# Optimization experiments

Measured on AMD Instinct MI355X. Metric: run time of the kernel, lower is better.

## Reference

```python
import jax, jax.numpy as jnp
import numpy as np

HID, HEADS = 1024, 16
HEAD_DIM = HID // HEADS

def _rope_table(seq_len, d):
    inv_freq = 1.0 / (10000.0 ** (jnp.arange(0, d, 2, dtype=jnp.float32) / d))  # [d/2]
    sin_inp = jnp.arange(seq_len, dtype=jnp.float32)[:, None] * inv_freq[None, :]  # [S, d/2]
    return jnp.concatenate([jnp.sin(sin_inp), jnp.cos(sin_inp)], axis=-1)  # [S, d]

def _apply_rope(x, pos_emb):
    # Faithful to original: cos/sin of the (already sin/cos) pos_emb values.
    half = x.shape[-1] // 2
    x1, x2 = x[..., :half], x[..., half:]
    p1, p2 = pos_emb[..., :half], pos_emb[..., half:]
    return jnp.concatenate([x1 * jnp.cos(p1) + x2 * jnp.sin(p1),
                            x2 * jnp.cos(p2) - x1 * jnp.sin(p2)], axis=-1)

def setup_inputs() -> dict:
    key = jax.random.key(0)
    ks = jax.random.split(key, 11)
    B, S = 8, 1024
    s = 1.0 / np.sqrt(HID)
    return {
        'query': jax.random.normal(ks[0], (B, S, HID), jnp.float32),
        'key':   jax.random.normal(ks[1], (B, S, HID), jnp.float32),
        'value': jax.random.normal(ks[2], (B, S, HID), jnp.float32),
        'Wq': jax.random.normal(ks[3], (HID, HID), jnp.float32) * s,
        'bq': jax.random.normal(ks[4], (HID,), jnp.float32) * s,
        'Wk': jax.random.normal(ks[5], (HID, HID), jnp.float32) * s,
        'bk': jax.random.normal(ks[6], (HID,), jnp.float32) * s,
        'Wv': jax.random.normal(ks[7], (HID, HID), jnp.float32) * s,
        'bv': jax.random.normal(ks[8], (HID,), jnp.float32) * s,
        'Wo': jax.random.normal(ks[9], (HID, HID), jnp.float32) * s,
        'bo': jax.random.normal(ks[10], (HID,), jnp.float32) * s,
    }

def reference(query, key, value, Wq, bq, Wk, bk, Wv, bv, Wo, bo):
    B, S, _ = query.shape
    q = query @ Wq.T + bq
    k = key @ Wk.T + bk
    v = value @ Wv.T + bv
    pos_emb = _rope_table(S, HID)
    q = _apply_rope(q, pos_emb)
    k = _apply_rope(k, pos_emb)
    v = _apply_rope(v, pos_emb)  # original applies RoPE to V too
    # split heads: [B, H, S, D]
    q = q.reshape(B, S, HEADS, HEAD_DIM).transpose(0, 2, 1, 3)
    k = k.reshape(B, S, HEADS, HEAD_DIM).transpose(0, 2, 1, 3)
    v = v.reshape(B, S, HEADS, HEAD_DIM).transpose(0, 2, 1, 3)
    scale = jnp.sqrt(jnp.float32(HEAD_DIM))
    attn = jnp.einsum('bhqd,bhkd->bhqk', q, k) / scale
    attn = jax.nn.softmax(attn, axis=-1)  # dropout=0.0 (eval): identity
    x = jnp.einsum('bhqk,bhkd->bhqd', attn, v)
    x = x.transpose(0, 2, 1, 3).reshape(B, S, HID)
    return x @ Wo.T + bo
```

## Files before the change

### kernel.cpp

```cpp
#include <hip/hip_runtime.h>
#include <hip/hip_fp16.h>
#include <cmath>


typedef _Float16 f16;
typedef __attribute__((ext_vector_type(4))) _Float16 f16x4;
typedef __attribute__((ext_vector_type(8))) _Float16 f16x8;
typedef __attribute__((ext_vector_type(4))) float f32x4;

#define MFMA16(a, b, c) __builtin_amdgcn_mfma_f32_16x16x32_f16((a), (b), (c), 0, 0, 0)
#define MFMA16K16(a, b, c) __builtin_amdgcn_mfma_f32_16x16x16f16((a), (b), (c), 0, 0, 0)

__device__ __forceinline__ void g2l16(void* lds, const void* g) {
  __builtin_amdgcn_global_load_lds(
      (const __attribute__((address_space(1))) void*)g,
      (__attribute__((address_space(3))) void*)lds,
      16, 0, 0);
}

__global__ void cvt3_kernel(const float* __restrict__ a, const float* __restrict__ b,
                            const float* __restrict__ c,
                            f16* __restrict__ oa, f16* __restrict__ ob, f16* __restrict__ oc) {
  const float* src;
  f16* dst;
  if (blockIdx.y == 0) { src = a; dst = oa; }
  else if (blockIdx.y == 1) { src = b; dst = ob; }
  else { src = c; dst = oc; }
  size_t t = (size_t)blockIdx.x * 256 + threadIdx.x;
  float4 v = ((const float4*)src)[t];
  f16x4 w = { (f16)v.x, (f16)v.y, (f16)v.z, (f16)v.w };
  ((f16x4*)dst)[t] = w;
}

__global__ void cvt4_kernel(const float* __restrict__ a, const float* __restrict__ b,
                            const float* __restrict__ c, const float* __restrict__ d,
                            f16* __restrict__ oa, f16* __restrict__ ob,
                            f16* __restrict__ oc, f16* __restrict__ od) {
  const float* src;
  f16* dst;
  if (blockIdx.y == 0) { src = a; dst = oa; }
  else if (blockIdx.y == 1) { src = b; dst = ob; }
  else if (blockIdx.y == 2) { src = c; dst = oc; }
  else { src = d; dst = od; }
  size_t t = (size_t)blockIdx.x * 256 + threadIdx.x;
  float4 v = ((const float4*)src)[t];
  f16x4 w = { (f16)v.x, (f16)v.y, (f16)v.z, (f16)v.w };
  ((f16x4*)dst)[t] = w;
}

struct GemmBatch {
  const f16* A[3];
  const f16* W[3];
  const float* bias[3];
  void* O[3];
};

template <bool OUT_F16>
__global__ __launch_bounds__(256)
void gemm_f16_kernel(GemmBatch gb) {
  __shared__ __align__(16) f16 sA[128 * 64];
  __shared__ __align__(16) f16 sB[128 * 64];
  const int z = blockIdx.z;
  const f16* __restrict__ A = gb.A[z];
  const f16* __restrict__ Bw = gb.W[z];
  const float* __restrict__ bias = gb.bias[z];
  void* __restrict__ Out = gb.O[z];

  const int tid = threadIdx.x;
  const int lane = tid & 63;
  const int wv = tid >> 6;
  const int l15 = lane & 15;
  const int quad = lane >> 4;
  const int m0 = blockIdx.y * 128;
  const int n0 = blockIdx.x * 128;

  const int srow = lane >> 3;
  const int schunk = (lane & 7) ^ srow;
  const int wm = (wv & 1) * 64;
  const int wn = (wv >> 1) * 64;

  const f16* gA = A + (size_t)(m0 + wv * 32 + srow) * 1024 + schunk * 8;
  const f16* gB = Bw + (size_t)(n0 + wv * 32 + srow) * 1024 + schunk * 8;
  f16* lA = sA + (wv * 32) * 64;
  f16* lB = sB + (wv * 32) * 64;

  f32x4 acc[4][4] = {};

  for (int k0 = 0; k0 < 1024; k0 += 64) {
    __syncthreads();
#pragma unroll
    for (int j = 0; j < 4; ++j) {
      g2l16(lA + j * 8 * 64, gA + (size_t)j * 8 * 1024 + k0);
      g2l16(lB + j * 8 * 64, gB + (size_t)j * 8 * 1024 + k0);
    }
    __syncthreads();
#pragma unroll
    for (int kc = 0; kc < 2; ++kc) {
      f16x8 af[4], bf[4];
#pragma unroll
      for (int t = 0; t < 4; ++t) {
        const int swz = ((kc * 4 + quad) ^ (l15 & 7)) * 8;
        af[t] = *(const f16x8*)(sA + (wm + t * 16 + l15) * 64 + swz);
        bf[t] = *(const f16x8*)(sB + (wn + t * 16 + l15) * 64 + swz);
      }
#pragma unroll
      for (int mi = 0; mi < 4; ++mi)
#pragma unroll
        for (int ni = 0; ni < 4; ++ni)
          acc[mi][ni] = MFMA16(af[mi], bf[ni], acc[mi][ni]);
    }
  }

#pragma unroll
  for (int ni = 0; ni < 4; ++ni) {
    const int col = n0 + wn + ni * 16 + l15;
    const float bv = bias[col];
#pragma unroll
    for (int mi = 0; mi < 4; ++mi) {
      const int row0 = m0 + wm + mi * 16 + quad * 4;
#pragma unroll
      for (int r = 0; r < 4; ++r) {
        float v = acc[mi][ni][r] + bv;
        if (OUT_F16)
          ((f16*)Out)[(size_t)(row0 + r) * 1024 + col] = (f16)v;
        else
          ((float*)Out)[(size_t)(row0 + r) * 1024 + col] = v;
      }
    }
  }
}

__global__ __launch_bounds__(256)
void rope_kernel(f16* __restrict__ q, f16* __restrict__ k,
                 const f16* __restrict__ v, f16* __restrict__ vt) {
  __shared__ f16 sT[128 * 72];
  const int t = threadIdx.x;
  const int c0 = blockIdx.x * 64;
  const int s0 = blockIdx.y * 64;
  const int b = blockIdx.z;
  const int sr = t >> 2;
  const int cq = (t & 3) * 16;
  const int s = s0 + sr;

  float c1[16], s1[16], c2[16], s2[16];
#pragma unroll
  for (int j = 0; j < 16; ++j) {
    const int i = c0 + cq + j;
    const float invf = exp2f((float)i * -0.025952563241307517f);
    const float th = (float)s * invf;
    const float p1 = sinf(th), p2 = cosf(th);
    c1[j] = __cosf(p1); s1[j] = __sinf(p1);
    c2[j] = __cosf(p2); s2[j] = __sinf(p2);
  }

  const size_t base = ((size_t)(b * 1024 + s)) * 1024 + c0 + cq;

#pragma unroll
  for (int tz = 0; tz < 2; ++tz) {
    f16* ptr = tz ? k : q;
    f16x8 x1a = *(f16x8*)(ptr + base);
    f16x8 x1b = *(f16x8*)(ptr + base + 8);
    f16x8 x2a = *(f16x8*)(ptr + base + 512);
    f16x8 x2b = *(f16x8*)(ptr + base + 520);
    f16x8 r1a, r1b, r2a, r2b;
#pragma unroll
    for (int j = 0; j < 8; ++j) {
      float a0 = (float)x1a[j], b0 = (float)x2a[j];
      float a1 = (float)x1b[j], b1 = (float)x2b[j];
      r1a[j] = (f16)(a0 * c1[j] + b0 * s1[j]);
      r2a[j] = (f16)(b0 * c2[j] - a0 * s2[j]);
      r1b[j] = (f16)(a1 * c1[8 + j] + b1 * s1[8 + j]);
      r2b[j] = (f16)(b1 * c2[8 + j] - a1 * s2[8 + j]);
    }
    *(f16x8*)(ptr + base) = r1a;
    *(f16x8*)(ptr + base + 8) = r1b;
    *(f16x8*)(ptr + base + 512) = r2a;
    *(f16x8*)(ptr + base + 520) = r2b;
  }

  {
    f16x8 x1a = *(const f16x8*)(v + base);
    f16x8 x1b = *(const f16x8*)(v + base + 8);
    f16x8 x2a = *(const f16x8*)(v + base + 512);
    f16x8 x2b = *(const f16x8*)(v + base + 520);
#pragma unroll
    for (int j = 0; j < 8; ++j) {
      float a0 = (float)x1a[j], b0 = (float)x2a[j];
      float a1 = (float)x1b[j], b1 = (float)x2b[j];
      sT[(cq + j) * 72 + sr] = (f16)(a0 * c1[j] + b0 * s1[j]);
      sT[(64 + cq + j) * 72 + sr] = (f16)(b0 * c2[j] - a0 * s2[j]);
      sT[(cq + 8 + j) * 72 + sr] = (f16)(a1 * c1[8 + j] + b1 * s1[8 + j]);
      sT[(64 + cq + 8 + j) * 72 + sr] = (f16)(b1 * c2[8 + j] - a1 * s2[8 + j]);
    }
  }
  __syncthreads();

  const int lr = t >> 1;
  const int sh = (t & 1) * 32;
  const int h = (lr < 64) ? (c0 >> 6) : (8 + (c0 >> 6));
  const int d = lr & 63;
  const size_t gbase = ((size_t)((b * 16 + h) * 64 + d)) * 1024 + s0 + sh;
#pragma unroll
  for (int m = 0; m < 4; ++m)
    *(f16x8*)(vt + gbase + m * 8) = *(const f16x8*)(sT + lr * 72 + sh + m * 8);
}

__global__ __launch_bounds__(256)
void attn_kernel(const f16* __restrict__ q, const f16* __restrict__ k,
                 const f16* __restrict__ vt, f16* __restrict__ xo) {
  __shared__ __align__(16) f16 sK[128 * 64];
  __shared__ __align__(16) f16 sV[64 * 128];
  const int tid = threadIdx.x;
  const int lane = tid & 63;
  const int wv = tid >> 6;
  const int l15 = lane & 15;
  const int quad = lane >> 4;
  const int bh = blockIdx.x;
  const int qt = blockIdx.y;
  const int b = bh >> 4, h = bh & 15;
  const size_t hidbase = ((size_t)b << 20) + (size_t)(h << 6);
  const int sq0 = qt * 128 + wv * 32;

  f16x8 fq[2][2];
#pragma unroll
  for (int mi = 0; mi < 2; ++mi)
#pragma unroll
    for (int kc = 0; kc < 2; ++kc)
      fq[mi][kc] = *(const f16x8*)(q + hidbase + (size_t)(sq0 + mi * 16 + l15) * 1024 +
                                   kc * 32 + quad * 8);

  f32x4 ot[2][4] = {};
  float lrun[2] = {};

  const float SC = 0.18033688011112042f;

  const int srowK = lane >> 3;
  const int schunkK = (lane & 7) ^ srowK;
  const f16* gK = k + hidbase + (size_t)(wv * 32 + srowK) * 1024 + schunkK * 8;
  const int vrow = lane >> 4;
  const f16* gVbase = vt + ((size_t)bh * 64) * 1024;

  for (int kt = 0; kt < 8; ++kt) {
    const int sk0 = kt * 128;
    __syncthreads();
#pragma unroll
    for (int j = 0; j < 4; ++j)
      g2l16(sK + (wv * 32 + j * 8) * 64, gK + (size_t)(sk0 + j * 8) * 1024);
#pragma unroll
    for (int i = 0; i < 4; ++i) {
      const int row = wv * 16 + i * 4 + vrow;
      const int gch = (lane & 15) ^ (i * 4 + vrow);
      g2l16(sV + (wv * 16 + i * 4) * 128, gVbase + (size_t)row * 1024 + sk0 + gch * 8);
    }
    __syncthreads();

#pragma unroll
    for (int nj = 0; nj < 8; ++nj) {
      f32x4 st[2] = {};
#pragma unroll
      for (int kc = 0; kc < 2; ++kc) {
        f16x8 fk = *(const f16x8*)(sK + (nj * 16 + l15) * 64 +
                                   ((kc * 4 + quad) ^ (l15 & 7)) * 8);
        st[0] = MFMA16(fk, fq[0][kc], st[0]);
        st[1] = MFMA16(fk, fq[1][kc], st[1]);
      }
      f16x4 pf[2];
#pragma unroll
      for (int mi = 0; mi < 2; ++mi) {
#pragma unroll
        for (int r = 0; r < 4; ++r) {
          float p = exp2f(fmaf(st[mi][r], SC, -12.0f));
          lrun[mi] += p;
          pf[mi][r] = (f16)p;
        }
      }
#pragma unroll
      for (int nd = 0; nd < 4; ++nd) {
        f16x4 fv = *(const f16x4*)(sV + (nd * 16 + l15) * 128 +
                                   ((nj * 2 + (quad >> 1)) ^ l15) * 8 + (quad & 1) * 4);
        ot[0][nd] = MFMA16K16(fv, pf[0], ot[0][nd]);
        ot[1][nd] = MFMA16K16(fv, pf[1], ot[1][nd]);
      }
    }
  }

  float inv[2];
#pragma unroll
  for (int mi = 0; mi < 2; ++mi) {
    float l = lrun[mi];
    l += __shfl_xor(l, 16, 64);
    l += __shfl_xor(l, 32, 64);
    inv[mi] = 1.0f / l;
  }

  __syncthreads();
  f16* sO = sK + wv * (32 * 72);
#pragma unroll
  for (int mi = 0; mi < 2; ++mi)
#pragma unroll
    for (int nd = 0; nd < 4; ++nd) {
      f16x4 w;
#pragma unroll
      for (int r = 0; r < 4; ++r) w[r] = (f16)(ot[mi][nd][r] * inv[mi]);
      *(f16x4*)(sO + (mi * 16 + l15) * 72 + nd * 16 + quad * 4) = w;
    }
  const int orow = lane >> 1;
  const int ocol = (lane & 1) * 32;
  const size_t gb = hidbase + (size_t)(sq0 + orow) * 1024 + ocol;
#pragma unroll
  for (int m = 0; m < 4; ++m)
    *(f16x8*)(xo + gb + m * 8) = *(const f16x8*)(sO + orow * 72 + ocol + m * 8);
}

extern "C" void kernel_launch(void* const* d_in, const int* in_sizes, int n_in,
                              void* d_out, int out_size, void* d_ws, size_t ws_size,
                              hipStream_t stream) {
  const float* query = (const float*)d_in[0];
  const float* key   = (const float*)d_in[1];
  const float* value = (const float*)d_in[2];
  const float* Wq = (const float*)d_in[3];
  const float* bq = (const float*)d_in[4];
  const float* Wk = (const float*)d_in[5];
  const float* bk = (const float*)d_in[6];
  const float* Wv = (const float*)d_in[7];
  const float* bv = (const float*)d_in[8];
  const float* Wo = (const float*)d_in[9];
  const float* bo = (const float*)d_in[10];

  char* ws = (char*)d_ws;
  const size_t SZT = (size_t)8 * 1024 * 1024 * 2;
  const size_t SZW = (size_t)1024 * 1024 * 2;
  f16* Xq  = (f16*)(ws);
  f16* Xk  = (f16*)(ws + SZT);
  f16* Xv  = (f16*)(ws + 2 * SZT);
  f16* Wqh = (f16*)(ws + 3 * SZT);
  f16* Wkh = (f16*)(ws + 3 * SZT + SZW);
  f16* Wvh = (f16*)(ws + 3 * SZT + 2 * SZW);
  f16* Woh = (f16*)(ws + 3 * SZT + 3 * SZW);
  f16* Qp  = (f16*)(ws + 3 * SZT + 4 * SZW);
  f16* Kp  = (f16*)(ws + 4 * SZT + 4 * SZW);
  f16* Vp  = (f16*)(ws + 5 * SZT + 4 * SZW);
  f16* Vt  = (f16*)(ws + 6 * SZT + 4 * SZW);
  f16* Xat = (f16*)(ws + 7 * SZT + 4 * SZW);

  cvt3_kernel<<<dim3(8192, 3), 256, 0, stream>>>(query, key, value, Xq, Xk, Xv);
  cvt4_kernel<<<dim3(1024, 4), 256, 0, stream>>>(Wq, Wk, Wv, Wo, Wqh, Wkh, Wvh, Woh);

  GemmBatch gqkv;
  gqkv.A[0] = Xq;  gqkv.A[1] = Xk;  gqkv.A[2] = Xv;
  gqkv.W[0] = Wqh; gqkv.W[1] = Wkh; gqkv.W[2] = Wvh;
  gqkv.bias[0] = bq; gqkv.bias[1] = bk; gqkv.bias[2] = bv;
  gqkv.O[0] = Qp;  gqkv.O[1] = Kp;  gqkv.O[2] = Vp;
  gemm_f16_kernel<true><<<dim3(8, 64, 3), 256, 0, stream>>>(gqkv);

  rope_kernel<<<dim3(8, 16, 8), 256, 0, stream>>>(Qp, Kp, Vp, Vt);

  attn_kernel<<<dim3(128, 8), 256, 0, stream>>>(Qp, Kp, Vt, Xat);

  GemmBatch go;
  go.A[0] = Xat; go.A[1] = nullptr; go.A[2] = nullptr;
  go.W[0] = Woh; go.W[1] = nullptr; go.W[2] = nullptr;
  go.bias[0] = bo; go.bias[1] = nullptr; go.bias[2] = nullptr;
  go.O[0] = d_out; go.O[1] = nullptr; go.O[2] = nullptr;
  gemm_f16_kernel<false><<<dim3(8, 64, 1), 256, 0, stream>>>(go);
}
```

Baseline: 341.9 us.

## Fuse fp32-to-fp16 activation conversion into QKV GEMM and remap tiles per XCD

Removes the separate conversion kernel for query/key/value. The QKV GEMM now loads fp32 activations directly, converts them in registers and stores swizzled fp16 into LDS, which saves writing and re-reading three fp16 activation copies. It also remaps the block index so that neighbouring M tiles are grouped per XCD, aiming for better L2 reuse. The cost is that A loads become synchronous register loads instead of async global-to-LDS loads, and each A byte is fetched at twice the width from global memory for every N tile.

```diff
diff --git a/kernel.cpp b/kernel.cpp
--- a/kernel.cpp
+++ b/kernel.cpp
@@ -16,20 +16,6 @@
       (const __attribute__((address_space(1))) void*)g,
       (__attribute__((address_space(3))) void*)lds,
       16, 0, 0);
-}
-
-__global__ void cvt3_kernel(const float* __restrict__ a, const float* __restrict__ b,
-                            const float* __restrict__ c,
-                            f16* __restrict__ oa, f16* __restrict__ ob, f16* __restrict__ oc) {
-  const float* src;
-  f16* dst;
-  if (blockIdx.y == 0) { src = a; dst = oa; }
-  else if (blockIdx.y == 1) { src = b; dst = ob; }
-  else { src = c; dst = oc; }
-  size_t t = (size_t)blockIdx.x * 256 + threadIdx.x;
-  float4 v = ((const float4*)src)[t];
-  f16x4 w = { (f16)v.x, (f16)v.y, (f16)v.z, (f16)v.w };
-  ((f16x4*)dst)[t] = w;
 }
 
 __global__ void cvt4_kernel(const float* __restrict__ a, const float* __restrict__ b,
@@ -49,19 +35,19 @@
 }
 
 struct GemmBatch {
-  const f16* A[3];
+  const void* A[3];
   const f16* W[3];
   const float* bias[3];
   void* O[3];
 };
 
-template <bool OUT_F16>
+template <bool A_FP32, bool OUT_F16>
 __global__ __launch_bounds__(256)
 void gemm_f16_kernel(GemmBatch gb) {
   __shared__ __align__(16) f16 sA[128 * 64];
   __shared__ __align__(16) f16 sB[128 * 64];
   const int z = blockIdx.z;
-  const f16* __restrict__ A = gb.A[z];
+  const void* __restrict__ Araw = gb.A[z];
   const f16* __restrict__ Bw = gb.W[z];
   const float* __restrict__ bias = gb.bias[z];
   void* __restrict__ Out = gb.O[z];
@@ -71,27 +57,57 @@
   const int wv = tid >> 6;
   const int l15 = lane & 15;
   const int quad = lane >> 4;
-  const int m0 = blockIdx.y * 128;
-  const int n0 = blockIdx.x * 128;
+
+  const int flat = blockIdx.x + (blockIdx.y << 3);
+  const int xcd = flat & 7;
+  const int t64 = flat >> 3;
+  const int m0 = (xcd * 8 + (t64 & 7)) * 128;
+  const int n0 = (t64 >> 3) * 128;
+
+  const int wm = (wv & 1) * 64;
+  const int wn = (wv >> 1) * 64;
 
   const int srow = lane >> 3;
   const int schunk = (lane & 7) ^ srow;
-  const int wm = (wv & 1) * 64;
-  const int wn = (wv >> 1) * 64;
-
-  const f16* gA = A + (size_t)(m0 + wv * 32 + srow) * 1024 + schunk * 8;
   const f16* gB = Bw + (size_t)(n0 + wv * 32 + srow) * 1024 + schunk * 8;
+  f16* lB = sB + (wv * 32) * 64;
+
+  const f16* gA16 = (const f16*)Araw + (size_t)(m0 + wv * 32 + srow) * 1024 + schunk * 8;
   f16* lA = sA + (wv * 32) * 64;
-  f16* lB = sB + (wv * 32) * 64;
+  const int gi = lane >> 4, ii = lane & 15;
+  const int rowl = gi * 8 + (ii >> 1);
+  const int kh = (ii & 1) * 32;
+  const float* gA32 = (const float*)Araw + (size_t)(m0 + wv * 32 + rowl) * 1024 + kh;
+  f16* sAw = sA + (size_t)(wv * 32 + rowl) * 64;
 
   f32x4 acc[4][4] = {};
 
   for (int k0 = 0; k0 < 1024; k0 += 64) {
     __syncthreads();
 #pragma unroll
-    for (int j = 0; j < 4; ++j) {
-      g2l16(lA + j * 8 * 64, gA + (size_t)j * 8 * 1024 + k0);
+    for (int j = 0; j < 4; ++j)
       g2l16(lB + j * 8 * 64, gB + (size_t)j * 8 * 1024 + k0);
+    if constexpr (A_FP32) {
+#pragma unroll
+      for (int half = 0; half < 2; ++half) {
+        float4 va[4];
+#pragma unroll
+        for (int j = 0; j < 4; ++j)
+          va[j] = *(const float4*)(gA32 + k0 + half * 16 + j * 4);
+        const float* vf = (const float*)va;
+#pragma unroll
+        for (int c = 0; c < 2; ++c) {
+          f16x8 w;
+#pragma unroll
+          for (int e = 0; e < 8; ++e) w[e] = (f16)vf[c * 8 + e];
+          const int ch = (ii & 1) * 4 + half * 2 + c;
+          *(f16x8*)(sAw + ((ch ^ (rowl & 7)) * 8)) = w;
+        }
+      }
+    } else {
+#pragma unroll
+      for (int j = 0; j < 4; ++j)
+        g2l16(lA + j * 8 * 64, gA16 + (size_t)j * 8 * 1024 + k0);
     }
     __syncthreads();
 #pragma unroll
@@ -330,28 +346,24 @@
   char* ws = (char*)d_ws;
   const size_t SZT = (size_t)8 * 1024 * 1024 * 2;
   const size_t SZW = (size_t)1024 * 1024 * 2;
-  f16* Xq  = (f16*)(ws);
-  f16* Xk  = (f16*)(ws + SZT);
-  f16* Xv  = (f16*)(ws + 2 * SZT);
-  f16* Wqh = (f16*)(ws + 3 * SZT);
-  f16* Wkh = (f16*)(ws + 3 * SZT + SZW);
-  f16* Wvh = (f16*)(ws + 3 * SZT + 2 * SZW);
-  f16* Woh = (f16*)(ws + 3 * SZT + 3 * SZW);
-  f16* Qp  = (f16*)(ws + 3 * SZT + 4 * SZW);
-  f16* Kp  = (f16*)(ws + 4 * SZT + 4 * SZW);
-  f16* Vp  = (f16*)(ws + 5 * SZT + 4 * SZW);
-  f16* Vt  = (f16*)(ws + 6 * SZT + 4 * SZW);
-  f16* Xat = (f16*)(ws + 7 * SZT + 4 * SZW);
-
-  cvt3_kernel<<<dim3(8192, 3), 256, 0, stream>>>(query, key, value, Xq, Xk, Xv);
+  f16* Wqh = (f16*)(ws);
+  f16* Wkh = (f16*)(ws + SZW);
+  f16* Wvh = (f16*)(ws + 2 * SZW);
+  f16* Woh = (f16*)(ws + 3 * SZW);
+  f16* Qp  = (f16*)(ws + 4 * SZW);
+  f16* Kp  = (f16*)(ws + 4 * SZW + SZT);
+  f16* Vp  = (f16*)(ws + 4 * SZW + 2 * SZT);
+  f16* Vt  = (f16*)(ws + 4 * SZW + 3 * SZT);
+  f16* Xat = (f16*)(ws + 4 * SZW + 4 * SZT);
+
   cvt4_kernel<<<dim3(1024, 4), 256, 0, stream>>>(Wq, Wk, Wv, Wo, Wqh, Wkh, Wvh, Woh);
 
   GemmBatch gqkv;
-  gqkv.A[0] = Xq;  gqkv.A[1] = Xk;  gqkv.A[2] = Xv;
-  gqkv.W[0] = Wqh; gqkv.W[1] = Wkh; gqkv.W[2] = Wvh;
+  gqkv.A[0] = query; gqkv.A[1] = key; gqkv.A[2] = value;
+  gqkv.W[0] = Wqh;   gqkv.W[1] = Wkh; gqkv.W[2] = Wvh;
   gqkv.bias[0] = bq; gqkv.bias[1] = bk; gqkv.bias[2] = bv;
-  gqkv.O[0] = Qp;  gqkv.O[1] = Kp;  gqkv.O[2] = Vp;
-  gemm_f16_kernel<true><<<dim3(8, 64, 3), 256, 0, stream>>>(gqkv);
+  gqkv.O[0] = Qp;    gqkv.O[1] = Kp;  gqkv.O[2] = Vp;
+  gemm_f16_kernel<true, true><<<dim3(8, 64, 3), 256, 0, stream>>>(gqkv);
 
   rope_kernel<<<dim3(8, 16, 8), 256, 0, stream>>>(Qp, Kp, Vp, Vt);
 
@@ -362,5 +374,5 @@
   go.W[0] = Woh; go.W[1] = nullptr; go.W[2] = nullptr;
   go.bias[0] = bo; go.bias[1] = nullptr; go.bias[2] = nullptr;
   go.O[0] = d_out; go.O[1] = nullptr; go.O[2] = nullptr;
-  gemm_f16_kernel<false><<<dim3(8, 64, 1), 256, 0, stream>>>(go);
-}
+  gemm_f16_kernel<false, false><<<dim3(8, 64, 1), 256, 0, stream>>>(go);
+}
```

After: 373.4 us. +9.2%, slower.
